# Kernel tuning notes

Measured on AMD Instinct MI355X. Metric: run time of the kernel, lower is better.

## Reference

```python
import jax, jax.numpy as jnp
import numpy as np

ALPHA = 0.2  # LeakyReLU negative slope


def setup_inputs() -> dict:
    key = jax.random.key(0)
    k1, k2, k3, k4 = jax.random.split(key, 4)
    B, N, F_IN, F_OUT = 4, 4096, 256, 256
    h = jax.random.normal(k1, (B, N, F_IN), dtype=jnp.float32)
    adj = jax.random.randint(k2, (B, N, N), 0, 2, dtype=jnp.int32)
    # xavier_normal with gain=1.414: std = gain*sqrt(2/(fan_in+fan_out))
    std_W = 1.414 * np.sqrt(2.0 / (F_IN + F_OUT))
    W = jax.random.normal(k3, (F_IN, F_OUT), dtype=jnp.float32) * std_W
    std_a = 1.414 * np.sqrt(2.0 / (1 + 2 * F_OUT))
    a = jax.random.normal(k4, (1, 2 * F_OUT), dtype=jnp.float32) * std_a
    return {"h": h, "adj": adj, "W": W, "a": a}


def reference(h, adj, W, a):
    # h: [B, N, F_in], adj: [B, N, N] (0/1), W: [F_in, F_out], a: [1, 2*F_out]
    F_out = W.shape[1]
    Hh = jnp.einsum('bni,io->bno', h, W)               # [B, N, F_out]
    a_src = a[0, :F_out]                                # attends to edge source i
    a_dst = a[0, F_out:]                                # attends to edge target j
    s = jnp.einsum('bno,o->bn', Hh, a_src)              # [B, N]
    d = jnp.einsum('bno,o->bn', Hh, a_dst)              # [B, N]
    # score(i,j) = a . concat(Hh_i, Hh_j) = s_i + d_j
    logits = s[:, :, None] + d[:, None, :]              # [B, N, N]
    # edge_e = exp(-leakyrelu(score)) only on edges (adj nonzero), else 0
    e = jnp.where(adj != 0,
                  jnp.exp(-jax.nn.leaky_relu(logits, negative_slope=ALPHA)),
                  jnp.zeros((), dtype=Hh.dtype))        # [B, N, N]
    rowsum = jnp.sum(e, axis=-1, keepdims=True)         # [B, N, 1]
    # rows with zero sum keep divisor 1 (as in the torch code)
    rowsum = jnp.where(rowsum == 0.0, 1.0, rowsum)
    h_prime = jnp.einsum('bnm,bmo->bno', e, Hh) / rowsum  # [B, N, F_out]
    return jax.nn.elu(h_prime)  # concat=True branch
```

## Files before the change

### kernel.cpp

```cpp
#include <hip/hip_runtime.h>

#define LRELU_ALPHA 0.2f

typedef __bf16 bf16x8 __attribute__((ext_vector_type(8)));
typedef unsigned short u16;
typedef unsigned short u16x8 __attribute__((ext_vector_type(8)));
typedef float f32x4 __attribute__((ext_vector_type(4)));
typedef int int4v __attribute__((ext_vector_type(4)));
typedef unsigned int u32;
typedef unsigned long long u64;

__device__ __forceinline__ u16 f2bf(float f) {
  unsigned int u = __float_as_uint(f);
  u += 0x7fffu + ((u >> 16) & 1u);
  return (u16)(u >> 16);
}

__device__ __forceinline__ void gload16(const void* g, void* lds) {
  __builtin_amdgcn_global_load_lds(
      (const __attribute__((address_space(1))) void*)g,
      (__attribute__((address_space(3))) void*)lds, 16, 0, 0);
}

__global__ __launch_bounds__(256) void packw(const int* __restrict__ adj,
                                             u32* __restrict__ maskg,
                                             const float* __restrict__ W,
                                             u16* __restrict__ WbT) {
  const int tid = threadIdx.x;
  if (blockIdx.x >= 4096) {
    int idx = (blockIdx.x - 4096) * 256 + tid;
    WbT[idx] = f2bf(W[(idx & 255) * 256 + (idx >> 8)]);
    return;
  }
  const int l = tid & 63, w = tid >> 6;
  const size_t row = (size_t)blockIdx.x * 4 + w;
  const int* arow = adj + row * 4096;
  u64* mrow = (u64*)(maskg + row * 128);
  for (int it = 0; it < 16; ++it) {
    const int* base = arow + it * 256;
    int v0 = base[l], v1 = base[l + 64], v2 = base[l + 128], v3 = base[l + 192];
    u64 b0 = __ballot(v0 != 0);
    u64 b1 = __ballot(v1 != 0);
    u64 b2 = __ballot(v2 != 0);
    u64 b3 = __ballot(v3 != 0);
    if (l == 0) {
      mrow[it * 4 + 0] = b0;
      mrow[it * 4 + 1] = b1;
      mrow[it * 4 + 2] = b2;
      mrow[it * 4 + 3] = b3;
    }
  }
}

__global__ __launch_bounds__(256) void gemm1(const float* __restrict__ h,
                                             const u16* __restrict__ WbT,
                                             const float* __restrict__ a,
                                             u16* __restrict__ HhTt,
                                             float* __restrict__ sbuf,
                                             float* __restrict__ dbuf) {
  const int tid = threadIdx.x, bid = blockIdx.x;
  const int l = tid & 63, w = tid >> 6;
  const int lr = l & 15;
  const int lk = (l >> 4) << 3;
  const int rowA = bid * 64 + 16 * w + lr;
  const float* hrow = h + (size_t)rowA * 256 + lk;

  f32x4 acc[16];
#pragma unroll
  for (int n = 0; n < 16; ++n) acc[n] = (f32x4){0.f, 0.f, 0.f, 0.f};

  for (int k0 = 0; k0 < 256; k0 += 32) {
    f32x4 a0 = *(const f32x4*)(hrow + k0);
    f32x4 a1 = *(const f32x4*)(hrow + k0 + 4);
    u16x8 au;
    au[0] = f2bf(a0[0]); au[1] = f2bf(a0[1]); au[2] = f2bf(a0[2]); au[3] = f2bf(a0[3]);
    au[4] = f2bf(a1[0]); au[5] = f2bf(a1[1]); au[6] = f2bf(a1[2]); au[7] = f2bf(a1[3]);
    bf16x8 af = __builtin_bit_cast(bf16x8, au);
#pragma unroll
    for (int n = 0; n < 16; ++n) {
      int4v bv = *(const int4v*)(WbT + (size_t)(16 * n + lr) * 256 + k0 + lk);
      bf16x8 bf = __builtin_bit_cast(bf16x8, bv);
      acc[n] = __builtin_amdgcn_mfma_f32_16x16x32_bf16(af, bf, acc[n], 0, 0, 0);
    }
  }

  float sp[4] = {0.f, 0.f, 0.f, 0.f}, dp[4] = {0.f, 0.f, 0.f, 0.f};
#pragma unroll
  for (int n = 0; n < 16; ++n) {
    int col = 16 * n + lr;
    float as = a[col];
    float ad = a[256 + col];
#pragma unroll
    for (int rr = 0; rr < 4; ++rr) {
      int row = bid * 64 + 16 * w + ((l >> 4) << 2) + rr;
      int bb = row >> 12, kk = row & 4095;
      float v = acc[n][rr];
      size_t addr = (size_t)bb * 1048576 + (size_t)(kk >> 5) * 8192 +
                    (col >> 4) * 512 + ((kk >> 3) & 3) * 128 + (col & 15) * 8 +
                    (kk & 7);
      HhTt[addr] = f2bf(v);
      sp[rr] += v * as;
      dp[rr] += v * ad;
    }
  }
#pragma unroll
  for (int rr = 0; rr < 4; ++rr) {
#pragma unroll
    for (int off = 1; off < 16; off <<= 1) {
      sp[rr] += __shfl_xor(sp[rr], off);
      dp[rr] += __shfl_xor(dp[rr], off);
    }
  }
  if ((l & 15) == 0) {
#pragma unroll
    for (int rr = 0; rr < 4; ++rr) {
      int row = bid * 64 + 16 * w + ((l >> 4) << 2) + rr;
      sbuf[row] = sp[rr];
      dbuf[row] = dp[rr];
    }
  }
}

__global__ __launch_bounds__(256, 2) void gat_main(const u32* __restrict__ maskg,
                                                   const u16* __restrict__ HhTt,
                                                   const float* __restrict__ s,
                                                   const float* __restrict__ d,
                                                   float* __restrict__ out) {
  __shared__ __align__(16) u16 Bt[3][4096];
  __shared__ __align__(16) u16 At[2][2048];
  __shared__ __align__(16) u32 Mk[8192];
  __shared__ __align__(16) float Dt[3][32];
  __shared__ float rs_lds[64];

  const int tid = threadIdx.x, bid = blockIdx.x;
  const int xcd = bid & 7;
  const int t = ((xcd & 1) << 6) | (bid >> 3);
  const int b = xcd >> 1;
  const int rowpanel = t >> 1, ch = t & 1;
  const int rowbase = rowpanel << 6;

  const int l = tid & 63, w = tid >> 6;
  const int lr = l & 15, lkg = l >> 4;
  const int wr = w & 1, wc = w >> 1;
  const int er = tid >> 2, c4 = tid & 3;

  {
    const u32* mrow = maskg + ((size_t)(b * 4096 + rowbase)) * 128;
    const int r = tid >> 2;
    const int w0 = (tid & 3) * 32;
#pragma unroll
    for (int j = 0; j < 32; ++j) {
      int ww = w0 + j;
      Mk[r * 128 + ((ww + r) & 127)] = mrow[r * 128 + ww];
    }
  }

  const float s_e = s[b * 4096 + rowbase + er];

  const char* bsrcB = (const char*)HhTt + (size_t)b * 2097152 + ch * 8192 + l * 16;
  const char* dsrcB = (const char*)d + (size_t)b * 16384 + w * 32 + l * 16;
  char* BtB = (char*)&Bt[0][0];
  char* DtB = (char*)&Dt[0][0];

  const int atoff0 = (32 * wr + lr) * 32 + lkg * 8;
  const int atoff1 = (32 * wr + 16 + lr) * 32 + lkg * 8;
  const int btbase = 4 * wc * 512 + lkg * 128 + lr * 8;

  f32x4 acc0[4], acc1[4];
#pragma unroll
  for (int n = 0; n < 4; ++n) {
    acc0[n] = (f32x4){0.f, 0.f, 0.f, 0.f};
    acc1[n] = (f32x4){0.f, 0.f, 0.f, 0.f};
  }
  float racc = 0.f;

#define ISSUE_B(BUF, STEP)                                                    \
  {                                                                           \
    const size_t so_ = (size_t)(STEP) * 16384;                                \
    gload16(bsrcB + so_ + (w * 2 + 0) * 1024,                                 \
            BtB + (BUF) * 8192 + (w * 2 + 0) * 1024);                         \
    gload16(bsrcB + so_ + (w * 2 + 1) * 1024,                                 \
            BtB + (BUF) * 8192 + (w * 2 + 1) * 1024);                         \
  }

#define ISSUE_D(STEP)                                                         \
  {                                                                           \
    const int dst_ = (STEP) > 127 ? 127 : (STEP);                             \
    if (l < 2) gload16(dsrcB + (size_t)dst_ * 128,                            \
                       DtB + (dst_ % 3) * 128 + w * 32 + l * 16);             \
  }

#define EGEN(BA, STEP)                                                        \
  {                                                                           \
    u32 mword = Mk[er * 128 + (((STEP) + er) & 127)];                         \
    u32 m8 = mword >> (c4 * 8);                                               \
    f32x4 dvA = *(const f32x4*)(DtB + ((STEP) % 3) * 128 + c4 * 32);          \
    f32x4 dvB = *(const f32x4*)(DtB + ((STEP) % 3) * 128 + c4 * 32 + 16);     \
    u16x8 ev;                                                                 \
    _Pragma("unroll")                                                         \
    for (int j = 0; j < 8; ++j) {                                             \
      float lg = s_e + (j < 4 ? dvA[j & 3] : dvB[j & 3]);                     \
      float tt = fmaxf(lg, LRELU_ALPHA * lg);                                 \
      float e = ((m8 >> j) & 1) ? __expf(-tt) : 0.f;                          \
      racc += e;                                                              \
      ev[j] = f2bf(e);                                                        \
    }                                                                         \
    *(int4v*)&At[BA][er * 32 + c4 * 8] = __builtin_bit_cast(int4v, ev);       \
  }

#define COMPUTE(BB, BA)                                                       \
  {                                                                           \
    bf16x8 af0 = __builtin_bit_cast(bf16x8, *(const int4v*)&At[BA][atoff0]);  \
    bf16x8 af1 = __builtin_bit_cast(bf16x8, *(const int4v*)&At[BA][atoff1]);  \
    __builtin_amdgcn_s_setprio(1);                                            \
    _Pragma("unroll")                                                         \
    for (int n = 0; n < 4; ++n) {                                             \
      bf16x8 bfv = __builtin_bit_cast(bf16x8,                                 \
          *(const int4v*)&Bt[BB][btbase + n * 512]);                          \
      acc0[n] = __builtin_amdgcn_mfma_f32_16x16x32_bf16(af0, bfv, acc0[n],    \
                                                        0, 0, 0);             \
      acc1[n] = __builtin_amdgcn_mfma_f32_16x16x32_bf16(af1, bfv, acc1[n],    \
                                                        0, 0, 0);             \
    }                                                                         \
    __builtin_amdgcn_s_setprio(0);                                            \
  }

#define SUBSTEP(J, BB, BA, BI, BAN)                                           \
  {                                                                           \
    ISSUE_B(BI, (J) + 2)                                                      \
    ISSUE_D((J) + 3)                                                          \
    EGEN(BAN, (J) + 1)                                                        \
    COMPUTE(BB, BA)                                                           \
    asm volatile("s_waitcnt lgkmcnt(0)" ::: "memory");                        \
    asm volatile("s_waitcnt vmcnt(3)" ::: "memory");                          \
    __builtin_amdgcn_s_barrier();                                             \
  }

  ISSUE_B(0, 0)
  ISSUE_B(1, 1)
  ISSUE_D(1)
  ISSUE_D(2)
  f32x4 d0A = *(const f32x4*)(d + b * 4096 + c4 * 8);
  f32x4 d0B = *(const f32x4*)(d + b * 4096 + c4 * 8 + 4);
  __syncthreads();
  {
    u32 mword = Mk[er * 128 + (er & 127)];
    u32 m8 = mword >> (c4 * 8);
    u16x8 ev;
#pragma unroll
    for (int j = 0; j < 8; ++j) {
      float lg = s_e + (j < 4 ? d0A[j & 3] : d0B[j & 3]);
      float tt = fmaxf(lg, LRELU_ALPHA * lg);
      float e = ((m8 >> j) & 1) ? __expf(-tt) : 0.f;
      racc += e;
      ev[j] = f2bf(e);
    }
    *(int4v*)&At[0][er * 32 + c4 * 8] = __builtin_bit_cast(int4v, ev);
  }
  asm volatile("s_waitcnt lgkmcnt(0)" ::: "memory");
  __builtin_amdgcn_s_barrier();

  for (int k = 0; k < 126; k += 6) {
    SUBSTEP(k + 0, 0, 0, 2, 1)
    SUBSTEP(k + 1, 1, 1, 0, 0)
    SUBSTEP(k + 2, 2, 0, 1, 1)
    SUBSTEP(k + 3, 0, 1, 2, 0)
    SUBSTEP(k + 4, 1, 0, 0, 1)
    SUBSTEP(k + 5, 2, 1, 1, 0)
  }
  EGEN(1, 127)
  COMPUTE(0, 0)
  asm volatile("s_waitcnt lgkmcnt(0)" ::: "memory");
  asm volatile("s_waitcnt vmcnt(0)" ::: "memory");
  __builtin_amdgcn_s_barrier();
  COMPUTE(1, 1)
#undef ISSUE_B
#undef ISSUE_D
#undef EGEN
#undef COMPUTE
#undef SUBSTEP

  racc += __shfl_xor(racc, 1);
  racc += __shfl_xor(racc, 2);
  if (c4 == 0) rs_lds[er] = (racc == 0.f) ? 1.f : racc;
  __syncthreads();

#pragma unroll
  for (int t16 = 0; t16 < 2; ++t16) {
#pragma unroll
    for (int n = 0; n < 4; ++n) {
#pragma unroll
      for (int reg = 0; reg < 4; ++reg) {
        int rloc = 32 * wr + 16 * t16 + lkg * 4 + reg;
        int col = ch * 128 + wc * 64 + 16 * n + lr;
        float v = (t16 ? acc1[n][reg] : acc0[n][reg]) / rs_lds[rloc];
        out[((size_t)(b * 4096 + rowbase + rloc)) * 256 + col] =
            v > 0.f ? v : (__expf(v) - 1.f);
      }
    }
  }
}

extern "C" void kernel_launch(void* const* d_in, const int* in_sizes, int n_in,
                              void* d_out, int out_size, void* d_ws, size_t ws_size,
                              hipStream_t stream) {
  const float* h = (const float*)d_in[0];
  const int* adj = (const int*)d_in[1];
  const float* W = (const float*)d_in[2];
  const float* a = (const float*)d_in[3];
  float* out = (float*)d_out;

  u16* WbT   = (u16*)d_ws;
  u16* HhTt  = (u16*)((char*)d_ws + 131072);
  float* sb  = (float*)((char*)d_ws + 131072 + 8388608);
  float* db  = sb + 16384;
  u32* maskg = (u32*)((char*)d_ws + 131072 + 8388608 + 131072);

  hipLaunchKernelGGL(packw,    dim3(4352), dim3(256), 0, stream, adj, maskg, W, WbT);
  hipLaunchKernelGGL(gemm1,    dim3(256),  dim3(256), 0, stream, h, WbT, a, HhTt, sb, db);
  hipLaunchKernelGGL(gat_main, dim3(512),  dim3(256), 0, stream, maskg, HhTt, sb, db, out);
}
```

Before: 173.9 us.

## Restructure GAT main kernel to register-resident attention tiles with direct global B loads

Replaces the LDS-staged, triple-buffered pipeline with a simpler scheme. Each block now covers 32 rows by all 256 output columns. Each wave computes its attention coefficients directly in MFMA A-operand registers, packs them with v_cvt_pk_bf16_f32, and loads the B operand (Hh) straight from global memory into registers. This removes the LDS round trip for A and B, the per-step barriers and the row-sum reduction through LDS, and puts the whole d vector in LDS. In exchange, Hh is loaded with no explicit prefetch, each block reads all 256 columns, and exp work is duplicated across the waves that share rows, so performance depends on L2 hits and latency hiding through occupancy.

```diff
diff --git a/kernel.cpp b/kernel.cpp
--- a/kernel.cpp
+++ b/kernel.cpp
@@ -8,18 +8,13 @@
 typedef float f32x4 __attribute__((ext_vector_type(4)));
 typedef int int4v __attribute__((ext_vector_type(4)));
 typedef unsigned int u32;
+typedef unsigned int u32x4 __attribute__((ext_vector_type(4)));
 typedef unsigned long long u64;
 
 __device__ __forceinline__ u16 f2bf(float f) {
   unsigned int u = __float_as_uint(f);
   u += 0x7fffu + ((u >> 16) & 1u);
   return (u16)(u >> 16);
-}
-
-__device__ __forceinline__ void gload16(const void* g, void* lds) {
-  __builtin_amdgcn_global_load_lds(
-      (const __attribute__((address_space(1))) void*)g,
-      (__attribute__((address_space(3))) void*)lds, 16, 0, 0);
 }
 
 __global__ __launch_bounds__(256) void packw(const int* __restrict__ adj,
@@ -126,177 +121,94 @@
                                                    const float* __restrict__ s,
                                                    const float* __restrict__ d,
                                                    float* __restrict__ out) {
-  __shared__ __align__(16) u16 Bt[3][4096];
-  __shared__ __align__(16) u16 At[2][2048];
-  __shared__ __align__(16) u32 Mk[8192];
-  __shared__ __align__(16) float Dt[3][32];
-  __shared__ float rs_lds[64];
+  __shared__ __align__(16) u32 Mk[32 * 128];
+  __shared__ __align__(16) float Dl[4096];
 
   const int tid = threadIdx.x, bid = blockIdx.x;
   const int xcd = bid & 7;
-  const int t = ((xcd & 1) << 6) | (bid >> 3);
-  const int b = xcd >> 1;
-  const int rowpanel = t >> 1, ch = t & 1;
-  const int rowbase = rowpanel << 6;
+  const int t = (xcd << 6) | (bid >> 3);
+  const int b = t >> 7;
+  const int rowbase = (t & 127) << 5;
 
   const int l = tid & 63, w = tid >> 6;
   const int lr = l & 15, lkg = l >> 4;
   const int wr = w & 1, wc = w >> 1;
-  const int er = tid >> 2, c4 = tid & 3;
-
+  const int rowl = wr * 16 + lr;
+
+  for (int i = tid; i < 1024; i += 256)
+    *(f32x4*)&Dl[i * 4] = *(const f32x4*)(d + b * 4096 + i * 4);
   {
     const u32* mrow = maskg + ((size_t)(b * 4096 + rowbase)) * 128;
-    const int r = tid >> 2;
-    const int w0 = (tid & 3) * 32;
-#pragma unroll
-    for (int j = 0; j < 32; ++j) {
-      int ww = w0 + j;
-      Mk[r * 128 + ((ww + r) & 127)] = mrow[r * 128 + ww];
-    }
-  }
-
-  const float s_e = s[b * 4096 + rowbase + er];
-
-  const char* bsrcB = (const char*)HhTt + (size_t)b * 2097152 + ch * 8192 + l * 16;
-  const char* dsrcB = (const char*)d + (size_t)b * 16384 + w * 32 + l * 16;
-  char* BtB = (char*)&Bt[0][0];
-  char* DtB = (char*)&Dt[0][0];
-
-  const int atoff0 = (32 * wr + lr) * 32 + lkg * 8;
-  const int atoff1 = (32 * wr + 16 + lr) * 32 + lkg * 8;
-  const int btbase = 4 * wc * 512 + lkg * 128 + lr * 8;
-
-  f32x4 acc0[4], acc1[4];
-#pragma unroll
-  for (int n = 0; n < 4; ++n) {
-    acc0[n] = (f32x4){0.f, 0.f, 0.f, 0.f};
-    acc1[n] = (f32x4){0.f, 0.f, 0.f, 0.f};
-  }
+    const int r = tid >> 3, c0 = (tid & 7) * 16;
+#pragma unroll
+    for (int j = 0; j < 16; ++j) {
+      int c = c0 + j;
+      Mk[r * 128 + ((c + r) & 127)] = mrow[r * 128 + c];
+    }
+  }
+  const float s_row = s[b * 4096 + rowbase + rowl];
+  __syncthreads();
+
+  const char* bsrc = (const char*)HhTt +
+      ((size_t)b * 1048576 + (wc * 8) * 512 + lkg * 128 + lr * 8) * 2;
+
+  f32x4 acc[8];
+#pragma unroll
+  for (int n = 0; n < 8; ++n) acc[n] = (f32x4){0.f, 0.f, 0.f, 0.f};
   float racc = 0.f;
-
-#define ISSUE_B(BUF, STEP)                                                    \
-  {                                                                           \
-    const size_t so_ = (size_t)(STEP) * 16384;                                \
-    gload16(bsrcB + so_ + (w * 2 + 0) * 1024,                                 \
-            BtB + (BUF) * 8192 + (w * 2 + 0) * 1024);                         \
-    gload16(bsrcB + so_ + (w * 2 + 1) * 1024,                                 \
-            BtB + (BUF) * 8192 + (w * 2 + 1) * 1024);                         \
-  }
-
-#define ISSUE_D(STEP)                                                         \
-  {                                                                           \
-    const int dst_ = (STEP) > 127 ? 127 : (STEP);                             \
-    if (l < 2) gload16(dsrcB + (size_t)dst_ * 128,                            \
-                       DtB + (dst_ % 3) * 128 + w * 32 + l * 16);             \
-  }
-
-#define EGEN(BA, STEP)                                                        \
-  {                                                                           \
-    u32 mword = Mk[er * 128 + (((STEP) + er) & 127)];                         \
-    u32 m8 = mword >> (c4 * 8);                                               \
-    f32x4 dvA = *(const f32x4*)(DtB + ((STEP) % 3) * 128 + c4 * 32);          \
-    f32x4 dvB = *(const f32x4*)(DtB + ((STEP) % 3) * 128 + c4 * 32 + 16);     \
-    u16x8 ev;                                                                 \
-    _Pragma("unroll")                                                         \
-    for (int j = 0; j < 8; ++j) {                                             \
-      float lg = s_e + (j < 4 ? dvA[j & 3] : dvB[j & 3]);                     \
-      float tt = fmaxf(lg, LRELU_ALPHA * lg);                                 \
-      float e = ((m8 >> j) & 1) ? __expf(-tt) : 0.f;                          \
-      racc += e;                                                              \
-      ev[j] = f2bf(e);                                                        \
-    }                                                                         \
-    *(int4v*)&At[BA][er * 32 + c4 * 8] = __builtin_bit_cast(int4v, ev);       \
-  }
-
-#define COMPUTE(BB, BA)                                                       \
-  {                                                                           \
-    bf16x8 af0 = __builtin_bit_cast(bf16x8, *(const int4v*)&At[BA][atoff0]);  \
-    bf16x8 af1 = __builtin_bit_cast(bf16x8, *(const int4v*)&At[BA][atoff1]);  \
-    __builtin_amdgcn_s_setprio(1);                                            \
-    _Pragma("unroll")                                                         \
-    for (int n = 0; n < 4; ++n) {                                             \
-      bf16x8 bfv = __builtin_bit_cast(bf16x8,                                 \
-          *(const int4v*)&Bt[BB][btbase + n * 512]);                          \
-      acc0[n] = __builtin_amdgcn_mfma_f32_16x16x32_bf16(af0, bfv, acc0[n],    \
-                                                        0, 0, 0);             \
-      acc1[n] = __builtin_amdgcn_mfma_f32_16x16x32_bf16(af1, bfv, acc1[n],    \
-                                                        0, 0, 0);             \
-    }                                                                         \
-    __builtin_amdgcn_s_setprio(0);                                            \
-  }
-
-#define SUBSTEP(J, BB, BA, BI, BAN)                                           \
-  {                                                                           \
-    ISSUE_B(BI, (J) + 2)                                                      \
-    ISSUE_D((J) + 3)                                                          \
-    EGEN(BAN, (J) + 1)                                                        \
-    COMPUTE(BB, BA)                                                           \
-    asm volatile("s_waitcnt lgkmcnt(0)" ::: "memory");                        \
-    asm volatile("s_waitcnt vmcnt(3)" ::: "memory");                          \
-    __builtin_amdgcn_s_barrier();                                             \
-  }
-
-  ISSUE_B(0, 0)
-  ISSUE_B(1, 1)
-  ISSUE_D(1)
-  ISSUE_D(2)
-  f32x4 d0A = *(const f32x4*)(d + b * 4096 + c4 * 8);
-  f32x4 d0B = *(const f32x4*)(d + b * 4096 + c4 * 8 + 4);
-  __syncthreads();
-  {
-    u32 mword = Mk[er * 128 + (er & 127)];
-    u32 m8 = mword >> (c4 * 8);
-    u16x8 ev;
+  const int mkbase = rowl * 128;
+
+  for (int step = 0; step < 128; ++step) {
+    const char* bs = bsrc + (size_t)step * 16384;
+    int4v bv[8];
+#pragma unroll
+    for (int n = 0; n < 8; ++n) bv[n] = *(const int4v*)(bs + n * 1024);
+
+    u32 mword = Mk[mkbase + ((step + rowl) & 127)];
+    u32 m8 = mword >> (lkg * 8);
+    f32x4 dA = *(const f32x4*)&Dl[step * 32 + lkg * 8];
+    f32x4 dB = *(const f32x4*)&Dl[step * 32 + lkg * 8 + 4];
+    float ev[8];
 #pragma unroll
     for (int j = 0; j < 8; ++j) {
-      float lg = s_e + (j < 4 ? d0A[j & 3] : d0B[j & 3]);
+      float lg = s_row + (j < 4 ? dA[j & 3] : dB[j & 3]);
       float tt = fmaxf(lg, LRELU_ALPHA * lg);
       float e = ((m8 >> j) & 1) ? __expf(-tt) : 0.f;
       racc += e;
-      ev[j] = f2bf(e);
-    }
-    *(int4v*)&At[0][er * 32 + c4 * 8] = __builtin_bit_cast(int4v, ev);
-  }
-  asm volatile("s_waitcnt lgkmcnt(0)" ::: "memory");
-  __builtin_amdgcn_s_barrier();
-
-  for (int k = 0; k < 126; k += 6) {
-    SUBSTEP(k + 0, 0, 0, 2, 1)
-    SUBSTEP(k + 1, 1, 1, 0, 0)
-    SUBSTEP(k + 2, 2, 0, 1, 1)
-    SUBSTEP(k + 3, 0, 1, 2, 0)
-    SUBSTEP(k + 4, 1, 0, 0, 1)
-    SUBSTEP(k + 5, 2, 1, 1, 0)
-  }
-  EGEN(1, 127)
-  COMPUTE(0, 0)
-  asm volatile("s_waitcnt lgkmcnt(0)" ::: "memory");
-  asm volatile("s_waitcnt vmcnt(0)" ::: "memory");
-  __builtin_amdgcn_s_barrier();
-  COMPUTE(1, 1)
-#undef ISSUE_B
-#undef ISSUE_D
-#undef EGEN
-#undef COMPUTE
-#undef SUBSTEP
-
-  racc += __shfl_xor(racc, 1);
-  racc += __shfl_xor(racc, 2);
-  if (c4 == 0) rs_lds[er] = (racc == 0.f) ? 1.f : racc;
-  __syncthreads();
-
-#pragma unroll
-  for (int t16 = 0; t16 < 2; ++t16) {
-#pragma unroll
-    for (int n = 0; n < 4; ++n) {
-#pragma unroll
-      for (int reg = 0; reg < 4; ++reg) {
-        int rloc = 32 * wr + 16 * t16 + lkg * 4 + reg;
-        int col = ch * 128 + wc * 64 + 16 * n + lr;
-        float v = (t16 ? acc1[n][reg] : acc0[n][reg]) / rs_lds[rloc];
-        out[((size_t)(b * 4096 + rowbase + rloc)) * 256 + col] =
-            v > 0.f ? v : (__expf(v) - 1.f);
-      }
+      ev[j] = e;
+    }
+    u32x4 pk;
+    asm("v_cvt_pk_bf16_f32 %0, %1, %2" : "=v"(pk[0]) : "v"(ev[0]), "v"(ev[1]));
+    asm("v_cvt_pk_bf16_f32 %0, %1, %2" : "=v"(pk[1]) : "v"(ev[2]), "v"(ev[3]));
+    asm("v_cvt_pk_bf16_f32 %0, %1, %2" : "=v"(pk[2]) : "v"(ev[4]), "v"(ev[5]));
+    asm("v_cvt_pk_bf16_f32 %0, %1, %2" : "=v"(pk[3]) : "v"(ev[6]), "v"(ev[7]));
+    bf16x8 af = __builtin_bit_cast(bf16x8, pk);
+
+#pragma unroll
+    for (int n = 0; n < 8; ++n) {
+      bf16x8 bfv = __builtin_bit_cast(bf16x8, bv[n]);
+      acc[n] = __builtin_amdgcn_mfma_f32_16x16x32_bf16(af, bfv, acc[n], 0, 0, 0);
+    }
+  }
+
+  racc += __shfl_xor(racc, 16);
+  racc += __shfl_xor(racc, 32);
+  float inv[4];
+#pragma unroll
+  for (int reg = 0; reg < 4; ++reg) {
+    float rsv = __shfl(racc, lkg * 4 + reg);
+    inv[reg] = 1.f / (rsv == 0.f ? 1.f : rsv);
+  }
+
+  const size_t obase =
+      ((size_t)(b * 4096 + rowbase + wr * 16 + lkg * 4)) * 256 + wc * 128;
+#pragma unroll
+  for (int n = 0; n < 8; ++n) {
+#pragma unroll
+    for (int reg = 0; reg < 4; ++reg) {
+      float v = acc[n][reg] * inv[reg];
+      out[obase + (size_t)reg * 256 + 16 * n + lr] =
+          v > 0.f ? v : (__expf(v) - 1.f);
     }
   }
 }
```

New measurement: 172.0 us. Within noise of the previous version (-1.1%).
